# Kernel tuning notes

Measured on AMD Instinct MI355X. Metric: run time of the kernel, lower is better.

Reference implementation:

```python
import jax, jax.numpy as jnp
import numpy as np

H = 512   # layer_size
D = 5     # dim
B = 64
T = 512
EPS = 1e-3  # Keras BatchNormalization default epsilon


def _p(key, shape, scale=0.05):
    return jax.random.normal(key, shape, dtype=jnp.float32) * scale


def setup_inputs() -> dict:
    key = jax.random.key(0)
    ks = jax.random.split(key, 32)
    inp = {
        "x": jax.random.normal(ks[0], (B, T, D), dtype=jnp.float32),
        # LSTM 1 (input D)
        "W1": _p(ks[1], (D, 4 * H)), "U1": _p(ks[2], (H, 4 * H)), "b1": jnp.zeros((4 * H,), jnp.float32),
        # BatchNorm on H features (inference: moving stats)
        "g1": jnp.ones((H,), jnp.float32), "be1": jnp.zeros((H,), jnp.float32),
        "m1": _p(ks[3], (H,), 0.1), "v1": jnp.ones((H,), jnp.float32) + jax.random.uniform(ks[4], (H,)) * 0.1,
        # LSTM 2 (input H)
        "W2": _p(ks[5], (H, 4 * H)), "U2": _p(ks[6], (H, 4 * H)), "b2": jnp.zeros((4 * H,), jnp.float32),
        # LSTM 3 (input H, returns last state only)
        "W3": _p(ks[7], (H, 4 * H)), "U3": _p(ks[8], (H, 4 * H)), "b3": jnp.zeros((4 * H,), jnp.float32),
        # dense head y
        "d1w": _p(ks[9], (H, 32)), "d1b": jnp.zeros((32,), jnp.float32),
        "g2": jnp.ones((32,), jnp.float32), "be2": jnp.zeros((32,), jnp.float32),
        "m2": _p(ks[10], (32,), 0.1), "v2": jnp.ones((32,), jnp.float32) + jax.random.uniform(ks[11], (32,)) * 0.1,
        "d2w": _p(ks[12], (32, 16)), "d2b": jnp.zeros((16,), jnp.float32),
        "hw": _p(ks[13], (16, 1)), "hb": jnp.zeros((1,), jnp.float32),
        # dense head z
        "d4w": _p(ks[14], (H, 128)), "d4b": jnp.zeros((128,), jnp.float32),
        "d5w": _p(ks[15], (128, 64)), "d5b": jnp.zeros((64,), jnp.float32),
        "rw": _p(ks[16], (64, D)), "rb": jnp.zeros((D,), jnp.float32),
    }
    return inp


def lstm(x, W, U, b):
    """Keras LSTM, gate order i,f,c,o. x: [B,T,din] -> (seq [B,T,H], h_T, c_T)."""
    xz = jnp.einsum('btd,dk->btk', x, W) + b  # precompute input projections [B,T,4H]

    def step(carry, xz_t):
        h, c = carry
        z = xz_t + h @ U
        i, f, g, o = jnp.split(z, 4, axis=-1)
        i = jax.nn.sigmoid(i)
        f = jax.nn.sigmoid(f)
        g = jnp.tanh(g)
        o = jax.nn.sigmoid(o)
        c = f * c + i * g
        h = o * jnp.tanh(c)
        return (h, c), h

    b_ = x.shape[0]
    h0 = jnp.zeros((b_, U.shape[0]), x.dtype)
    (hT, cT), hs = jax.lax.scan(step, (h0, h0), jnp.swapaxes(xz, 0, 1))
    return jnp.swapaxes(hs, 0, 1), hT, cT


def bn_inf(x, g, b, m, v):
    return (x - m) * (g / jnp.sqrt(v + EPS)) + b


def reference(x, W1, U1, b1, g1, be1, m1, v1, W2, U2, b2, W3, U3, b3,
              d1w, d1b, g2, be2, m2, v2, d2w, d2b, hw, hb,
              d4w, d4b, d5w, d5b, rw, rb):
    # inference: GaussianNoise / Dropout are identity
    x1, h1, s1 = lstm(x, W1, U1, b1)          # [B,T,H]
    xr = bn_inf(x1, g1, be1, m1, v1)
    x2, h2, s2 = lstm(xr, W2, U2, b2)         # [B,T,H]
    xs = x1 + x2                               # residual Add
    _, h3, s3 = lstm(xs, W3, U3, b3)           # last hidden state [B,H]
    xlast = h3
    # head y
    y = xlast @ d1w + d1b
    y = bn_inf(y, g2, be2, m2, v2)
    y = y @ d2w + d2b
    y = jax.nn.sigmoid(y @ hw + hb)            # [B,1]
    # head z
    z = xlast @ d4w + d4b
    z = z @ d5w + d5b
    z = z @ rw + rb                            # [B,D]
    return (y, z)
```

## Files before the change

### kernel.cpp

```cpp
#include <hip/hip_runtime.h>
#include <hip/hip_bf16.h>

typedef short bf16x8 __attribute__((ext_vector_type(8)));
typedef float f32x4 __attribute__((ext_vector_type(4)));
typedef unsigned short u16;
typedef unsigned int u32;
typedef unsigned long long u64;

#define EPSBN 1e-3f

__device__ __forceinline__ u16 f2b(float f){
  unsigned u = __float_as_uint(f);
  return (u16)((u + 0x7fffu + ((u >> 16) & 1u)) >> 16);
}
__device__ __forceinline__ float b2f(u16 v){ return __uint_as_float(((unsigned)v) << 16); }
__device__ __forceinline__ float sigm(float x){ return 1.f/(1.f + __expf(-x)); }
__device__ __forceinline__ float tanhx(float x){ return 2.f/(1.f + __expf(-2.f*x)) - 1.f; }

union U64x2 { u64 q[2]; bf16x8 v; };


__global__ void prep_sv(const float* __restrict__ g1, const float* __restrict__ be1,
                        const float* __restrict__ m1, const float* __restrict__ v1,
                        float* __restrict__ s, float* __restrict__ tv){
  int k = blockIdx.x*256 + threadIdx.x;
  if (k < 512){
    float sv = g1[k] * rsqrtf(v1[k] + EPSBN);
    s[k] = sv;
    tv[k] = be1[k] - m1[k]*sv;
  }
}

__global__ void prep_b2p(const float* __restrict__ W2, const float* __restrict__ b2,
                         const float* __restrict__ tv, float* __restrict__ out){
  int col = blockIdx.x*256 + threadIdx.x;
  float acc = b2[col];
  for (int k=0;k<512;++k) acc += tv[k] * W2[(size_t)k*2048 + col];
  out[col] = acc;
}

__global__ void transpose_pack(const float* __restrict__ in, const float* __restrict__ scale,
                               u16* __restrict__ out){
  __shared__ float tile[64][65];
  int k0 = blockIdx.x * 64;
  int c0 = blockIdx.y * 64;
  int t = threadIdx.x;
  int cc = t & 63, kk0 = (t >> 6) * 16;
  #pragma unroll
  for (int i=0;i<16;++i){
    float v = in[(size_t)(k0 + kk0 + i)*2048 + c0 + cc];
    if (scale) v *= scale[k0 + kk0 + i];
    tile[kk0 + i][cc] = v;
  }
  __syncthreads();
  int cc2 = t >> 2, kp = t & 3;
  int col = c0 + cc2;
  int hcol = col & 511;
  int row = (hcol >> 5)*128 + (col >> 9)*32 + ((hcol >> 4) & 1)*16 + (col & 15);
  bf16x8 v0, v1;
  #pragma unroll
  for (int i=0;i<8;++i){
    v0[i] = (short)f2b(tile[kp*16 + i][cc2]);
    v1[i] = (short)f2b(tile[kp*16 + 8 + i][cc2]);
  }
  u16* dst = out + (size_t)row*512 + k0 + kp*16;
  *(bf16x8*)dst = v0;
  *(bf16x8*)(dst + 8) = v1;
}

__global__ void pack_w1(const float* __restrict__ W1, u16* __restrict__ out){
  int r = blockIdx.x*256 + threadIdx.x;
  int wg = r >> 7, q = (r >> 5) & 3, jt = (r >> 4) & 1, jj = r & 15;
  int col = q*512 + wg*32 + jt*16 + jj;
  #pragma unroll
  for (int k=0;k<32;++k)
    out[(size_t)r*32 + k] = (k < 5) ? f2b(W1[(size_t)k*2048 + col]) : (u16)0;
}

__global__ void pack_x(const float* __restrict__ x, u16* __restrict__ out){
  int i = blockIdx.x*256 + threadIdx.x;
  int k = i & 31;
  int bt = i >> 5;
  out[i] = (k < 5) ? f2b(x[(size_t)bt*5 + k]) : (u16)0;
}

__global__ void __launch_bounds__(256, 1) scan_all(
    const u16* __restrict__ Ure1, const u16* __restrict__ Ure2, const u16* __restrict__ Ure3,
    const u16* __restrict__ W1p,  const u16* __restrict__ W2p,  const u16* __restrict__ W3p,
    const u16* __restrict__ xpad,
    const float* __restrict__ b1, const float* __restrict__ b2p, const float* __restrict__ b3,
    u32* __restrict__ hbuf_all,
    u32* __restrict__ x1seq,
    u32* __restrict__ xsseq,
    float* __restrict__ h3out, u32* __restrict__ cnt)
{
  const int bid = blockIdx.x;
  const int phase = bid >> 6;
  const int b6 = bid & 63;
  const int g = b6 & 3, wg = b6 >> 2;
  const int tid = threadIdx.x;
  const int w = tid >> 6, l = tid & 63;
  const int lm = l & 15, lh = l >> 4;
  const int bg0 = g * 16;
  const int b_own = tid & 15, jl = tid >> 4;
  const int pb = tid >> 4, pj = tid & 15;

  const u16* Ure  = phase == 0 ? Ure1 : (phase == 1 ? Ure2 : Ure3);
  const u16* Wre  = phase == 0 ? W1p  : (phase == 1 ? W2p  : W3p);
  const float* bias = phase == 0 ? b1 : (phase == 1 ? b2p : b3);
  u32* hbuf32 = hbuf_all + (size_t)phase * 32768;
  u32* seqout = phase == 0 ? x1seq : (phase == 1 ? xsseq : nullptr);
  const u32* upseq = phase == 1 ? x1seq : (phase == 2 ? xsseq : nullptr);

  u32* cq  = cnt + (phase*4 + g)*64;
  u32* sq_ = cq + 32;
  u32* upq = (phase > 0) ? cnt + ((phase-1)*4 + g)*64 + 32 : nullptr;

  bf16x8 aU[8][4];
  #pragma unroll
  for (int q=0;q<4;++q)
    #pragma unroll
    for (int jt=0;jt<2;++jt){
      const u16* up = Ure + (size_t)(wg*128 + q*32 + jt*16 + lm)*512 + w*128 + lh*8;
      #pragma unroll
      for (int ks=0;ks<4;++ks) aU[q*2+jt][ks] = *(const bf16x8*)(up + ks*32);
    }
  bf16x8 aW[8][4];
  if (phase == 0){
    #pragma unroll
    for (int q=0;q<4;++q)
      #pragma unroll
      for (int jt=0;jt<2;++jt)
        aW[q*2+jt][0] = *(const bf16x8*)(Wre + (size_t)(wg*128 + q*32 + jt*16 + lm)*32 + lh*8);
  } else {
    #pragma unroll
    for (int q=0;q<4;++q)
      #pragma unroll
      for (int jt=0;jt<2;++jt){
        const u16* wp = Wre + (size_t)(wg*128 + q*32 + jt*16 + lm)*512 + w*128 + lh*8;
        #pragma unroll
        for (int ks=0;ks<4;++ks) aW[q*2+jt][ks] = *(const bf16x8*)(wp + ks*32);
      }
  }

  float bias_g[4][2];
  #pragma unroll
  for (int q=0;q<4;++q){
    bias_g[q][0] = bias[q*512 + wg*32 + jl];
    bias_g[q][1] = bias[q*512 + wg*32 + jl + 16];
  }

  float cs0 = 0.f, cs1 = 0.f;

  __shared__ float zex[8][4][16][17];
  __shared__ __align__(8) u16 hsh[16][32];
  __shared__ __align__(8) u16 xsh[16][32];
  __shared__ u32 x1w[16][16];

  const u64* hbase = (const u64*)hbuf32;

  for (int t=0; t<512; ++t){
    f32x4 acc[8] = {};

    if (phase == 0){
      if (w == 0){
        bf16x8 bx = *(const bf16x8*)(xpad + ((size_t)(bg0+lm)*512 + t)*32 + lh*8);
        #pragma unroll
        for (int i=0;i<8;++i)
          acc[i] = __builtin_amdgcn_mfma_f32_16x16x32_bf16(aW[i][0], bx, acc[i], 0,0,0);
      }
    } else {
      if (tid == 0){
        const u32 target = (u32)(16*(t+1));
        while (__hip_atomic_load(upq, __ATOMIC_RELAXED, __HIP_MEMORY_SCOPE_AGENT) < target) {}
      }
      __syncthreads();
      if (phase == 1){
        u32 rv = __hip_atomic_load(upseq + ((size_t)(bg0+pb)*512 + t)*256 + wg*16 + pj,
                                   __ATOMIC_RELAXED, __HIP_MEMORY_SCOPE_AGENT);
        x1w[pb][pj] = rv;
      }
      const u64* xp = (const u64*)upseq + ((size_t)(bg0+lm)*512 + t)*128 + w*32 + lh*2;
      U64x2 xq[4];
      #pragma unroll
      for (int ks=0;ks<4;++ks){
        xq[ks].q[0] = __hip_atomic_load(xp + ks*8,     __ATOMIC_RELAXED, __HIP_MEMORY_SCOPE_AGENT);
        xq[ks].q[1] = __hip_atomic_load(xp + ks*8 + 1, __ATOMIC_RELAXED, __HIP_MEMORY_SCOPE_AGENT);
      }
      #pragma unroll
      for (int ks=0;ks<4;++ks){
        #pragma unroll
        for (int i=0;i<8;++i)
          acc[i] = __builtin_amdgcn_mfma_f32_16x16x32_bf16(aW[i][ks], xq[ks].v, acc[i], 0,0,0);
      }
    }

    if (tid == 0){
      const u32 target = (u32)(16*t);
      while (__hip_atomic_load(cq, __ATOMIC_RELAXED, __HIP_MEMORY_SCOPE_AGENT) < target) {}
    }
    __syncthreads();

    {
      const u64* hp = hbase + (size_t)(((t+1)&1)*64 + bg0 + lm)*128 + w*32 + lh*2;
      U64x2 hq[4];
      #pragma unroll
      for (int ks=0;ks<4;++ks){
        hq[ks].q[0] = __hip_atomic_load(hp + ks*8,     __ATOMIC_RELAXED, __HIP_MEMORY_SCOPE_AGENT);
        hq[ks].q[1] = __hip_atomic_load(hp + ks*8 + 1, __ATOMIC_RELAXED, __HIP_MEMORY_SCOPE_AGENT);
      }
      #pragma unroll
      for (int ks=0;ks<4;++ks){
        #pragma unroll
        for (int i=0;i<8;++i)
          acc[i] = __builtin_amdgcn_mfma_f32_16x16x32_bf16(aU[i][ks], hq[ks].v, acc[i], 0,0,0);
      }
    }

    #pragma unroll
    for (int i=0;i<8;++i){
      #pragma unroll
      for (int r=0;r<4;++r)
        zex[i][w][lh*4 + r][lm] = acc[i][r];
    }
    __syncthreads();

    float hv0, hv1;
    {
      float zv[4][2];
      #pragma unroll
      for (int q=0;q<4;++q){
        #pragma unroll
        for (int s2=0;s2<2;++s2)
          zv[q][s2] = zex[q*2+s2][0][jl][b_own] + zex[q*2+s2][1][jl][b_own]
                    + zex[q*2+s2][2][jl][b_own] + zex[q*2+s2][3][jl][b_own] + bias_g[q][s2];
      }
      float iv = sigm(zv[0][0]), fv = sigm(zv[1][0]), gv = tanhx(zv[2][0]), ov = sigm(zv[3][0]);
      cs0 = fv * cs0 + iv * gv;
      hv0 = ov * tanhx(cs0);
      iv = sigm(zv[0][1]); fv = sigm(zv[1][1]); gv = tanhx(zv[2][1]); ov = sigm(zv[3][1]);
      cs1 = fv * cs1 + iv * gv;
      hv1 = ov * tanhx(cs1);
    }

    hsh[b_own][jl]      = f2b(hv0);
    hsh[b_own][jl + 16] = f2b(hv1);
    if (phase == 1){
      u32 w0 = x1w[b_own][jl >> 1], w1 = x1w[b_own][8 + (jl >> 1)];
      float x1r0 = b2f((u16)((jl & 1) ? (w0 >> 16) : (w0 & 0xffffu)));
      float x1r1 = b2f((u16)((jl & 1) ? (w1 >> 16) : (w1 & 0xffffu)));
      xsh[b_own][jl]      = f2b(x1r0 + hv0);
      xsh[b_own][jl + 16] = f2b(x1r1 + hv1);
    }
    if (phase == 2 && t == 511){
      h3out[(size_t)(bg0+b_own)*512 + wg*32 + jl]      = hv0;
      h3out[(size_t)(bg0+b_own)*512 + wg*32 + jl + 16] = hv1;
    }
    __syncthreads();

    u32 pv = (u32)hsh[pb][2*pj] | ((u32)hsh[pb][2*pj+1] << 16);
    __hip_atomic_store(hbuf32 + (size_t)((t&1)*64 + bg0 + pb)*256 + wg*16 + pj, pv,
                       __ATOMIC_RELAXED, __HIP_MEMORY_SCOPE_AGENT);
    if (phase == 0){
      __hip_atomic_store(seqout + ((size_t)(bg0+pb)*512 + t)*256 + wg*16 + pj, pv,
                         __ATOMIC_RELAXED, __HIP_MEMORY_SCOPE_AGENT);
    } else if (phase == 1){
      u32 sv = (u32)xsh[pb][2*pj] | ((u32)xsh[pb][2*pj+1] << 16);
      __hip_atomic_store(seqout + ((size_t)(bg0+pb)*512 + t)*256 + wg*16 + pj, sv,
                         __ATOMIC_RELAXED, __HIP_MEMORY_SCOPE_AGENT);
    }
    asm volatile("s_waitcnt vmcnt(0)" ::: "memory");
    __syncthreads();
    if (tid == 0){
      __hip_atomic_fetch_add(cq, 1u, __ATOMIC_RELAXED, __HIP_MEMORY_SCOPE_AGENT);
      if (phase < 2)
        __hip_atomic_fetch_add(sq_, 1u, __ATOMIC_RELAXED, __HIP_MEMORY_SCOPE_AGENT);
    }
  }
}

__global__ void __launch_bounds__(256) head_k(
    const float* __restrict__ h3,
    const float* __restrict__ d1w, const float* __restrict__ d1b,
    const float* __restrict__ g2, const float* __restrict__ be2,
    const float* __restrict__ m2, const float* __restrict__ v2,
    const float* __restrict__ d2w, const float* __restrict__ d2b,
    const float* __restrict__ hw, const float* __restrict__ hb,
    const float* __restrict__ d4w, const float* __restrict__ d4b,
    const float* __restrict__ d5w, const float* __restrict__ d5b,
    const float* __restrict__ rw, const float* __restrict__ rb,
    float* __restrict__ out)
{
  __shared__ float hl[512];
  __shared__ float a1[32], a2[16], c1[128], c2[64];
  int b = blockIdx.x, t = threadIdx.x;
  for (int i=t; i<512; i+=256) hl[i] = h3[(size_t)b*512 + i];
  __syncthreads();
  if (t < 32){
    float acc = d1b[t];
    for (int k=0;k<512;++k) acc += hl[k] * d1w[(size_t)k*32 + t];
    a1[t] = (acc - m2[t]) * (g2[t] * rsqrtf(v2[t] + EPSBN)) + be2[t];
  } else if (t >= 128){
    int i = t - 128;
    float acc = d4b[i];
    for (int k=0;k<512;++k) acc += hl[k] * d4w[(size_t)k*128 + i];
    c1[i] = acc;
  }
  __syncthreads();
  if (t < 16){
    float acc = d2b[t];
    for (int k=0;k<32;++k) acc += a1[k] * d2w[k*16 + t];
    a2[t] = acc;
  } else if (t >= 64 && t < 128){
    int i = t - 64;
    float acc = d5b[i];
    for (int k=0;k<128;++k) acc += c1[k] * d5w[k*64 + i];
    c2[i] = acc;
  }
  __syncthreads();
  if (t == 0){
    float acc = hb[0];
    for (int k=0;k<16;++k) acc += a2[k] * hw[k];
    out[b] = 1.f/(1.f + __expf(-acc));
  } else if (t >= 32 && t < 37){
    int i = t - 32;
    float acc = rb[i];
    for (int k=0;k<64;++k) acc += c2[k] * rw[k*5 + i];
    out[64 + b*5 + i] = acc;
  }
}

extern "C" void kernel_launch(void* const* d_in, const int* in_sizes, int n_in,
                              void* d_out, int out_size, void* d_ws, size_t ws_size,
                              hipStream_t stream)
{
  const float* x   = (const float*)d_in[0];
  const float* W1  = (const float*)d_in[1];
  const float* U1  = (const float*)d_in[2];
  const float* b1  = (const float*)d_in[3];
  const float* g1  = (const float*)d_in[4];
  const float* be1 = (const float*)d_in[5];
  const float* m1  = (const float*)d_in[6];
  const float* v1  = (const float*)d_in[7];
  const float* W2  = (const float*)d_in[8];
  const float* U2  = (const float*)d_in[9];
  const float* b2  = (const float*)d_in[10];
  const float* W3  = (const float*)d_in[11];
  const float* U3  = (const float*)d_in[12];
  const float* b3  = (const float*)d_in[13];
  const float* d1w = (const float*)d_in[14];
  const float* d1b = (const float*)d_in[15];
  const float* g2  = (const float*)d_in[16];
  const float* be2 = (const float*)d_in[17];
  const float* m2  = (const float*)d_in[18];
  const float* v2  = (const float*)d_in[19];
  const float* d2w = (const float*)d_in[20];
  const float* d2b = (const float*)d_in[21];
  const float* hw  = (const float*)d_in[22];
  const float* hb  = (const float*)d_in[23];
  const float* d4w = (const float*)d_in[24];
  const float* d4b = (const float*)d_in[25];
  const float* d5w = (const float*)d_in[26];
  const float* d5b = (const float*)d_in[27];
  const float* rw  = (const float*)d_in[28];
  const float* rb  = (const float*)d_in[29];

  char* ws = (char*)d_ws;
  constexpr size_t SZ_W   = 2048ull*512*2;
  constexpr size_t o_Ure1 = 0;
  constexpr size_t o_Ure2 = o_Ure1 + SZ_W;
  constexpr size_t o_Ure3 = o_Ure2 + SZ_W;
  constexpr size_t o_W2p  = o_Ure3 + SZ_W;
  constexpr size_t o_W3p  = o_W2p + SZ_W;
  constexpr size_t o_W1p  = o_W3p + SZ_W;
  constexpr size_t o_xpad = o_W1p + 2048ull*32*2;
  constexpr size_t o_b2p  = o_xpad + 64ull*512*32*2;
  constexpr size_t o_s    = o_b2p + 2048ull*4;
  constexpr size_t o_tv   = o_s + 512ull*4;
  constexpr size_t o_h3   = o_tv + 512ull*4;
  constexpr size_t o_h    = o_h3 + 64ull*512*4;
  constexpr size_t SZ_HP  = 2ull*64*256*4;
  constexpr size_t SZ_H   = 3*SZ_HP;
  constexpr size_t o_cnt  = o_h + SZ_H;
  constexpr size_t SZ_CNT = 3ull*4*64*4;
  constexpr size_t o_x1   = o_cnt + 4096;
  constexpr size_t o_xs   = o_x1 + 64ull*512*512*2;

  u16* Ure1 = (u16*)(ws + o_Ure1);
  u16* Ure2 = (u16*)(ws + o_Ure2);
  u16* Ure3 = (u16*)(ws + o_Ure3);
  u16* W2p  = (u16*)(ws + o_W2p);
  u16* W3p  = (u16*)(ws + o_W3p);
  u16* W1p  = (u16*)(ws + o_W1p);
  u16* xpad = (u16*)(ws + o_xpad);
  u32* x1p  = (u32*)(ws + o_x1);
  u32* xsp  = (u32*)(ws + o_xs);

  hipMemsetAsync(ws + o_h, 0, SZ_H + SZ_CNT, stream);

  prep_sv<<<dim3(2), dim3(256), 0, stream>>>(g1, be1, m1, v1, (float*)(ws+o_s), (float*)(ws+o_tv));
  transpose_pack<<<dim3(8,32), dim3(256), 0, stream>>>(U1, nullptr, Ure1);
  transpose_pack<<<dim3(8,32), dim3(256), 0, stream>>>(U2, nullptr, Ure2);
  transpose_pack<<<dim3(8,32), dim3(256), 0, stream>>>(U3, nullptr, Ure3);
  transpose_pack<<<dim3(8,32), dim3(256), 0, stream>>>(W3, nullptr, W3p);
  transpose_pack<<<dim3(8,32), dim3(256), 0, stream>>>(W2, (const float*)(ws+o_s), W2p);
  prep_b2p<<<dim3(8), dim3(256), 0, stream>>>(W2, b2, (const float*)(ws+o_tv), (float*)(ws+o_b2p));
  pack_w1<<<dim3(8), dim3(256), 0, stream>>>(W1, W1p);
  pack_x<<<dim3(4096), dim3(256), 0, stream>>>(x, xpad);

  scan_all<<<dim3(192), dim3(256), 0, stream>>>(
      Ure1, Ure2, Ure3, W1p, W2p, W3p, xpad,
      b1, (const float*)(ws+o_b2p), b3,
      (u32*)(ws+o_h), x1p, xsp,
      (float*)(ws+o_h3), (u32*)(ws+o_cnt));

  head_k<<<dim3(64), dim3(256), 0, stream>>>((const float*)(ws+o_h3),
      d1w, d1b, g2, be2, m2, v2, d2w, d2b, hw, hb, d4w, d4b, d5w, d5b, rw, rb,
      (float*)d_out);
}
```

Baseline: 2.338 ms.

## Replace shared atomic counters with per-wave flag stores and wave-level polling

Replaces the single per-group atomic counter, which thread 0 incremented and polled behind workgroup barriers, with per-wave flag slots. Each wave stores its timestep and waits only on the specific flags whose data it reads, with all lanes polling in parallel under __all. This removes contended atomic read-modify-writes and two __syncthreads per step from the critical recurrence path. The risks are more polling traffic and subtle memory-ordering issues, since the stores are relaxed and the cross-wave dependency mapping must be exactly right.

```diff
diff --git a/kernel.cpp b/kernel.cpp
--- a/kernel.cpp
+++ b/kernel.cpp
@@ -84,6 +84,10 @@
   out[i] = (k < 5) ? f2b(x[(size_t)bt*5 + k]) : (u16)0;
 }
 
+__device__ __forceinline__ void poll_flags(const u32* p, u32 target, bool act){
+  while (!__all((!act) | (__hip_atomic_load(p, __ATOMIC_RELAXED, __HIP_MEMORY_SCOPE_AGENT) >= target))) {}
+}
+
 __global__ void __launch_bounds__(256, 1) scan_all(
     const u16* __restrict__ Ure1, const u16* __restrict__ Ure2, const u16* __restrict__ Ure3,
     const u16* __restrict__ W1p,  const u16* __restrict__ W2p,  const u16* __restrict__ W3p,
@@ -92,7 +96,7 @@
     u32* __restrict__ hbuf_all,
     u32* __restrict__ x1seq,
     u32* __restrict__ xsseq,
-    float* __restrict__ h3out, u32* __restrict__ cnt)
+    float* __restrict__ h3out, u32* __restrict__ flags_base)
 {
   const int bid = blockIdx.x;
   const int phase = bid >> 6;
@@ -112,9 +116,13 @@
   u32* seqout = phase == 0 ? x1seq : (phase == 1 ? xsseq : nullptr);
   const u32* upseq = phase == 1 ? x1seq : (phase == 2 ? xsseq : nullptr);
 
-  u32* cq  = cnt + (phase*4 + g)*64;
-  u32* sq_ = cq + 32;
-  u32* upq = (phase > 0) ? cnt + ((phase-1)*4 + g)*64 + 32 : nullptr;
+  u32* flg  = flags_base + (phase*4 + g)*64;
+  const u32* upflg = (phase > 0) ? flags_base + ((phase-1)*4 + g)*64 : nullptr;
+
+  const u32* hpoll = flg + 16*w + (l & 15);
+  const u32* xpoll = (phase > 0)
+      ? ((l < 16) ? upflg + 16*w + l : upflg + 4*wg + w)
+      : nullptr;
 
   bf16x8 aU[8][4];
   #pragma unroll
@@ -170,11 +178,7 @@
           acc[i] = __builtin_amdgcn_mfma_f32_16x16x32_bf16(aW[i][0], bx, acc[i], 0,0,0);
       }
     } else {
-      if (tid == 0){
-        const u32 target = (u32)(16*(t+1));
-        while (__hip_atomic_load(upq, __ATOMIC_RELAXED, __HIP_MEMORY_SCOPE_AGENT) < target) {}
-      }
-      __syncthreads();
+      poll_flags(xpoll, (u32)(t+1), l < 20);
       if (phase == 1){
         u32 rv = __hip_atomic_load(upseq + ((size_t)(bg0+pb)*512 + t)*256 + wg*16 + pj,
                                    __ATOMIC_RELAXED, __HIP_MEMORY_SCOPE_AGENT);
@@ -195,11 +199,7 @@
       }
     }
 
-    if (tid == 0){
-      const u32 target = (u32)(16*t);
-      while (__hip_atomic_load(cq, __ATOMIC_RELAXED, __HIP_MEMORY_SCOPE_AGENT) < target) {}
-    }
-    __syncthreads();
+    poll_flags(hpoll, (u32)t, true);
 
     {
       const u64* hp = hbase + (size_t)(((t+1)&1)*64 + bg0 + lm)*128 + w*32 + lh*2;
@@ -270,12 +270,9 @@
                          __ATOMIC_RELAXED, __HIP_MEMORY_SCOPE_AGENT);
     }
     asm volatile("s_waitcnt vmcnt(0)" ::: "memory");
-    __syncthreads();
-    if (tid == 0){
-      __hip_atomic_fetch_add(cq, 1u, __ATOMIC_RELAXED, __HIP_MEMORY_SCOPE_AGENT);
-      if (phase < 2)
-        __hip_atomic_fetch_add(sq_, 1u, __ATOMIC_RELAXED, __HIP_MEMORY_SCOPE_AGENT);
-    }
+    if (l == 0)
+      __hip_atomic_store(flg + wg*4 + w, (u32)(t+1),
+                         __ATOMIC_RELAXED, __HIP_MEMORY_SCOPE_AGENT);
   }
 }
 
```

Result: slower. 2.579 ms (+10.3%).

## Replace per-step counter barrier with tagged hidden-state words polled by consumers

Applied to the files above, without the earlier changes.

Each bf16 hidden value is now stored together with a 16-bit timestep tag in one 32-bit word. Consumer waves spin directly on the tagged data until every tag matches the expected step, which removes the intra-layer atomic counter wait, its syncthreads and the counter increment for the recurrent dependency. The counter and its fence are kept only for the cross-layer sequence handoff, and phase 2 drops them entirely. The cost is twice the h-buffer traffic and repeated polling reads. Shared arrays are also padded to change bank mapping.

```diff
diff --git a/kernel.cpp b/kernel.cpp
--- a/kernel.cpp
+++ b/kernel.cpp
@@ -18,6 +18,7 @@
 __device__ __forceinline__ float tanhx(float x){ return 2.f/(1.f + __expf(-2.f*x)) - 1.f; }
 
 union U64x2 { u64 q[2]; bf16x8 v; };
+union BP    { u32 p[4]; bf16x8 v; };
 
 
 __global__ void prep_sv(const float* __restrict__ g1, const float* __restrict__ be1,
@@ -108,13 +109,12 @@
   const u16* Ure  = phase == 0 ? Ure1 : (phase == 1 ? Ure2 : Ure3);
   const u16* Wre  = phase == 0 ? W1p  : (phase == 1 ? W2p  : W3p);
   const float* bias = phase == 0 ? b1 : (phase == 1 ? b2p : b3);
-  u32* hbuf32 = hbuf_all + (size_t)phase * 32768;
+  u32* hbuf32 = hbuf_all + (size_t)phase * 65536;
   u32* seqout = phase == 0 ? x1seq : (phase == 1 ? xsseq : nullptr);
   const u32* upseq = phase == 1 ? x1seq : (phase == 2 ? xsseq : nullptr);
 
   u32* cq  = cnt + (phase*4 + g)*64;
-  u32* sq_ = cq + 32;
-  u32* upq = (phase > 0) ? cnt + ((phase-1)*4 + g)*64 + 32 : nullptr;
+  const u32* upq = (phase > 0) ? cnt + ((phase-1)*4 + g)*64 : nullptr;
 
   bf16x8 aU[8][4];
   #pragma unroll
@@ -152,12 +152,12 @@
 
   float cs0 = 0.f, cs1 = 0.f;
 
-  __shared__ float zex[8][4][16][17];
-  __shared__ __align__(8) u16 hsh[16][32];
-  __shared__ __align__(8) u16 xsh[16][32];
-  __shared__ u32 x1w[16][16];
-
-  const u64* hbase = (const u64*)hbuf32;
+  __shared__ float zex[8][4][16][18];
+  __shared__ u16 hsh[16][34];
+  __shared__ u16 xsh[16][34];
+  __shared__ u32 x1w[16][17];
+
+  const u64 tagmask = 0x0000FFFF0000FFFFull;
 
   for (int t=0; t<512; ++t){
     f32x4 acc[8] = {};
@@ -195,25 +195,38 @@
       }
     }
 
-    if (tid == 0){
-      const u32 target = (u32)(16*t);
-      while (__hip_atomic_load(cq, __ATOMIC_RELAXED, __HIP_MEMORY_SCOPE_AGENT) < target) {}
-    }
-    __syncthreads();
-
-    {
-      const u64* hp = hbase + (size_t)(((t+1)&1)*64 + bg0 + lm)*128 + w*32 + lh*2;
-      U64x2 hq[4];
+    if (t > 0){
+      const int slot = (t+1) & 1;
+      const u64* hp = (const u64*)hbuf32
+                    + (size_t)(slot*64 + bg0 + lm)*256 + w*64 + lh*4;
+      const u32 tg = (u32)t;
+      const u64 want = (u64)tg | ((u64)tg << 32);
+      u64 raw[16];
+      bool ok;
+      do {
+        #pragma unroll
+        for (int ks=0;ks<4;++ks)
+          #pragma unroll
+          for (int qq=0;qq<4;++qq)
+            raw[ks*4+qq] = __hip_atomic_load(hp + ks*16 + qq,
+                                             __ATOMIC_RELAXED, __HIP_MEMORY_SCOPE_AGENT);
+        u64 bad = 0;
+        #pragma unroll
+        for (int i=0;i<16;++i) bad |= (raw[i] & tagmask) ^ want;
+        ok = __all(bad == 0);
+      } while (!ok);
       #pragma unroll
       for (int ks=0;ks<4;++ks){
-        hq[ks].q[0] = __hip_atomic_load(hp + ks*8,     __ATOMIC_RELAXED, __HIP_MEMORY_SCOPE_AGENT);
-        hq[ks].q[1] = __hip_atomic_load(hp + ks*8 + 1, __ATOMIC_RELAXED, __HIP_MEMORY_SCOPE_AGENT);
-      }
-      #pragma unroll
-      for (int ks=0;ks<4;++ks){
+        BP bp;
+        #pragma unroll
+        for (int qq=0;qq<4;++qq){
+          u32 lo = (u32)raw[ks*4+qq];
+          u32 hi = (u32)(raw[ks*4+qq] >> 32);
+          bp.p[qq] = (lo >> 16) | (hi & 0xFFFF0000u);
+        }
         #pragma unroll
         for (int i=0;i<8;++i)
-          acc[i] = __builtin_amdgcn_mfma_f32_16x16x32_bf16(aU[i][ks], hq[ks].v, acc[i], 0,0,0);
+          acc[i] = __builtin_amdgcn_mfma_f32_16x16x32_bf16(aU[i][ks], bp.v, acc[i], 0,0,0);
       }
     }
 
@@ -258,23 +271,26 @@
     }
     __syncthreads();
 
-    u32 pv = (u32)hsh[pb][2*pj] | ((u32)hsh[pb][2*pj+1] << 16);
-    __hip_atomic_store(hbuf32 + (size_t)((t&1)*64 + bg0 + pb)*256 + wg*16 + pj, pv,
-                       __ATOMIC_RELAXED, __HIP_MEMORY_SCOPE_AGENT);
-    if (phase == 0){
-      __hip_atomic_store(seqout + ((size_t)(bg0+pb)*512 + t)*256 + wg*16 + pj, pv,
+    {
+      const int pslot = t & 1;
+      const u32 tagv = (u32)(t + 1);
+      u32 w0 = ((u32)hsh[pb][2*pj]     << 16) | tagv;
+      u32 w1 = ((u32)hsh[pb][2*pj + 1] << 16) | tagv;
+      __hip_atomic_store((u64*)(hbuf32 + (size_t)(pslot*64 + bg0 + pb)*512 + wg*32) + pj,
+                         (u64)w0 | ((u64)w1 << 32),
                          __ATOMIC_RELAXED, __HIP_MEMORY_SCOPE_AGENT);
-    } else if (phase == 1){
-      u32 sv = (u32)xsh[pb][2*pj] | ((u32)xsh[pb][2*pj+1] << 16);
+    }
+
+    if (phase < 2){
+      u32 sv;
+      if (phase == 0) sv = (u32)hsh[pb][2*pj] | ((u32)hsh[pb][2*pj+1] << 16);
+      else            sv = (u32)xsh[pb][2*pj] | ((u32)xsh[pb][2*pj+1] << 16);
       __hip_atomic_store(seqout + ((size_t)(bg0+pb)*512 + t)*256 + wg*16 + pj, sv,
                          __ATOMIC_RELAXED, __HIP_MEMORY_SCOPE_AGENT);
-    }
-    asm volatile("s_waitcnt vmcnt(0)" ::: "memory");
-    __syncthreads();
-    if (tid == 0){
-      __hip_atomic_fetch_add(cq, 1u, __ATOMIC_RELAXED, __HIP_MEMORY_SCOPE_AGENT);
-      if (phase < 2)
-        __hip_atomic_fetch_add(sq_, 1u, __ATOMIC_RELAXED, __HIP_MEMORY_SCOPE_AGENT);
+      asm volatile("s_waitcnt vmcnt(0)" ::: "memory");
+      __syncthreads();
+      if (tid == 0)
+        __hip_atomic_fetch_add(cq, 1u, __ATOMIC_RELAXED, __HIP_MEMORY_SCOPE_AGENT);
     }
   }
 }
@@ -379,10 +395,9 @@
   constexpr size_t o_tv   = o_s + 512ull*4;
   constexpr size_t o_h3   = o_tv + 512ull*4;
   constexpr size_t o_h    = o_h3 + 64ull*512*4;
-  constexpr size_t SZ_HP  = 2ull*64*256*4;
+  constexpr size_t SZ_HP  = 2ull*64*512*4;
   constexpr size_t SZ_H   = 3*SZ_HP;
   constexpr size_t o_cnt  = o_h + SZ_H;
-  constexpr size_t SZ_CNT = 3ull*4*64*4;
   constexpr size_t o_x1   = o_cnt + 4096;
   constexpr size_t o_xs   = o_x1 + 64ull*512*512*2;
 
@@ -396,7 +411,7 @@
   u32* x1p  = (u32*)(ws + o_x1);
   u32* xsp  = (u32*)(ws + o_xs);
 
-  hipMemsetAsync(ws + o_h, 0, SZ_H + SZ_CNT, stream);
+  hipMemsetAsync(ws + o_h, 0, SZ_H + 4096, stream);
 
   prep_sv<<<dim3(2), dim3(256), 0, stream>>>(g1, be1, m1, v1, (float*)(ws+o_s), (float*)(ws+o_tv));
   transpose_pack<<<dim3(8,32), dim3(256), 0, stream>>>(U1, nullptr, Ure1);
```

Result: slower. 2.892 ms (+23.7%).

## Split LSTM scan blocks into eight waves and streamline cross-block signaling

Applied to the files above, without the earlier changes.

Each scan block now runs 512 threads (eight waves). Each wave handles one of the two j-tiles for one k-slice, so per-wave MFMA chains and register weight tiles are halved. All threads now poll the step counters directly instead of one thread polling before a barrier. The extra shared staging of h and xs is removed, and packed h, residual and sequence values are stored straight from the gate threads. The separate sequence counter and the explicit vmcnt wait before signaling are dropped. This shortens the per-step critical path, but it risks memory-ordering visibility issues and adds polling traffic from many lanes.

```diff
diff --git a/kernel.cpp b/kernel.cpp
--- a/kernel.cpp
+++ b/kernel.cpp
@@ -84,7 +84,11 @@
   out[i] = (k < 5) ? f2b(x[(size_t)bt*5 + k]) : (u16)0;
 }
 
-__global__ void __launch_bounds__(256, 1) scan_all(
+__device__ __forceinline__ void pollge(const u32* p, u32 target){
+  while (__hip_atomic_load(p, __ATOMIC_RELAXED, __HIP_MEMORY_SCOPE_AGENT) < target) {}
+}
+
+__global__ void __launch_bounds__(512, 2) scan_all(
     const u16* __restrict__ Ure1, const u16* __restrict__ Ure2, const u16* __restrict__ Ure3,
     const u16* __restrict__ W1p,  const u16* __restrict__ W2p,  const u16* __restrict__ W3p,
     const u16* __restrict__ xpad,
@@ -100,10 +104,11 @@
   const int g = b6 & 3, wg = b6 >> 2;
   const int tid = threadIdx.x;
   const int w = tid >> 6, l = tid & 63;
-  const int lm = l & 15, lh = l >> 4;
+  const int lm = l & 15, lh = (l >> 4) & 3;
+  const int kp = w & 3, jt = w >> 2;
   const int bg0 = g * 16;
-  const int b_own = tid & 15, jl = tid >> 4;
-  const int pb = tid >> 4, pj = tid & 15;
+  const int jp = tid & 15, gb = (tid >> 4) & 15;
+  const int jt2 = jp >> 3;
 
   const u16* Ure  = phase == 0 ? Ure1 : (phase == 1 ? Ure2 : Ure3);
   const u16* Wre  = phase == 0 ? W1p  : (phase == 1 ? W2p  : W3p);
@@ -113,74 +118,63 @@
   const u32* upseq = phase == 1 ? x1seq : (phase == 2 ? xsseq : nullptr);
 
   u32* cq  = cnt + (phase*4 + g)*64;
-  u32* sq_ = cq + 32;
-  u32* upq = (phase > 0) ? cnt + ((phase-1)*4 + g)*64 + 32 : nullptr;
-
-  bf16x8 aU[8][4];
+  const u32* upq = (phase > 0) ? cnt + ((phase-1)*4 + g)*64 : nullptr;
+
+  bf16x8 aU[4][4];
   #pragma unroll
-  for (int q=0;q<4;++q)
+  for (int q=0;q<4;++q){
+    const u16* up = Ure + (size_t)(wg*128 + q*32 + jt*16 + lm)*512 + kp*128 + lh*8;
     #pragma unroll
-    for (int jt=0;jt<2;++jt){
-      const u16* up = Ure + (size_t)(wg*128 + q*32 + jt*16 + lm)*512 + w*128 + lh*8;
-      #pragma unroll
-      for (int ks=0;ks<4;++ks) aU[q*2+jt][ks] = *(const bf16x8*)(up + ks*32);
-    }
-  bf16x8 aW[8][4];
+    for (int ks=0;ks<4;++ks) aU[q][ks] = *(const bf16x8*)(up + ks*32);
+  }
+  bf16x8 aW[4][4];
+  bf16x8 aW1[4];
   if (phase == 0){
-    #pragma unroll
-    for (int q=0;q<4;++q)
-      #pragma unroll
-      for (int jt=0;jt<2;++jt)
-        aW[q*2+jt][0] = *(const bf16x8*)(Wre + (size_t)(wg*128 + q*32 + jt*16 + lm)*32 + lh*8);
+    if (kp == 0){
+      #pragma unroll
+      for (int q=0;q<4;++q)
+        aW1[q] = *(const bf16x8*)(Wre + (size_t)(wg*128 + q*32 + jt*16 + lm)*32 + lh*8);
+    }
   } else {
     #pragma unroll
-    for (int q=0;q<4;++q)
-      #pragma unroll
-      for (int jt=0;jt<2;++jt){
-        const u16* wp = Wre + (size_t)(wg*128 + q*32 + jt*16 + lm)*512 + w*128 + lh*8;
-        #pragma unroll
-        for (int ks=0;ks<4;++ks) aW[q*2+jt][ks] = *(const bf16x8*)(wp + ks*32);
-      }
-  }
-
-  float bias_g[4][2];
-  #pragma unroll
-  for (int q=0;q<4;++q){
-    bias_g[q][0] = bias[q*512 + wg*32 + jl];
-    bias_g[q][1] = bias[q*512 + wg*32 + jl + 16];
+    for (int q=0;q<4;++q){
+      const u16* wp = Wre + (size_t)(wg*128 + q*32 + jt*16 + lm)*512 + kp*128 + lh*8;
+      #pragma unroll
+      for (int ks=0;ks<4;++ks) aW[q][ks] = *(const bf16x8*)(wp + ks*32);
+    }
+  }
+
+  float bias0[4], bias1[4];
+  if (tid < 256){
+    #pragma unroll
+    for (int q=0;q<4;++q){
+      bias0[q] = bias[q*512 + wg*32 + 2*jp];
+      bias1[q] = bias[q*512 + wg*32 + 2*jp + 1];
+    }
   }
 
   float cs0 = 0.f, cs1 = 0.f;
 
-  __shared__ float zex[8][4][16][17];
-  __shared__ __align__(8) u16 hsh[16][32];
-  __shared__ __align__(8) u16 xsh[16][32];
-  __shared__ u32 x1w[16][16];
-
+  __shared__ float zex[8][4][16][18];
   const u64* hbase = (const u64*)hbuf32;
 
   for (int t=0; t<512; ++t){
-    f32x4 acc[8] = {};
+    f32x4 acc[4] = {};
+    u32 rv = 0;
 
     if (phase == 0){
-      if (w == 0){
+      if (kp == 0){
         bf16x8 bx = *(const bf16x8*)(xpad + ((size_t)(bg0+lm)*512 + t)*32 + lh*8);
         #pragma unroll
-        for (int i=0;i<8;++i)
-          acc[i] = __builtin_amdgcn_mfma_f32_16x16x32_bf16(aW[i][0], bx, acc[i], 0,0,0);
+        for (int q=0;q<4;++q)
+          acc[q] = __builtin_amdgcn_mfma_f32_16x16x32_bf16(aW1[q], bx, acc[q], 0,0,0);
       }
     } else {
-      if (tid == 0){
-        const u32 target = (u32)(16*(t+1));
-        while (__hip_atomic_load(upq, __ATOMIC_RELAXED, __HIP_MEMORY_SCOPE_AGENT) < target) {}
-      }
-      __syncthreads();
-      if (phase == 1){
-        u32 rv = __hip_atomic_load(upseq + ((size_t)(bg0+pb)*512 + t)*256 + wg*16 + pj,
-                                   __ATOMIC_RELAXED, __HIP_MEMORY_SCOPE_AGENT);
-        x1w[pb][pj] = rv;
-      }
-      const u64* xp = (const u64*)upseq + ((size_t)(bg0+lm)*512 + t)*128 + w*32 + lh*2;
+      pollge(upq, (u32)(16*(t+1)));
+      if (phase == 1 && tid < 256)
+        rv = __hip_atomic_load(upseq + ((size_t)(bg0+gb)*512 + t)*256 + wg*16 + jp,
+                               __ATOMIC_RELAXED, __HIP_MEMORY_SCOPE_AGENT);
+      const u64* xp = (const u64*)upseq + ((size_t)(bg0+lm)*512 + t)*128 + kp*32 + lh*2;
       U64x2 xq[4];
       #pragma unroll
       for (int ks=0;ks<4;++ks){
@@ -190,19 +184,14 @@
       #pragma unroll
       for (int ks=0;ks<4;++ks){
         #pragma unroll
-        for (int i=0;i<8;++i)
-          acc[i] = __builtin_amdgcn_mfma_f32_16x16x32_bf16(aW[i][ks], xq[ks].v, acc[i], 0,0,0);
-      }
-    }
-
-    if (tid == 0){
-      const u32 target = (u32)(16*t);
-      while (__hip_atomic_load(cq, __ATOMIC_RELAXED, __HIP_MEMORY_SCOPE_AGENT) < target) {}
-    }
-    __syncthreads();
-
+        for (int q=0;q<4;++q)
+          acc[q] = __builtin_amdgcn_mfma_f32_16x16x32_bf16(aW[q][ks], xq[ks].v, acc[q], 0,0,0);
+      }
+    }
+
+    pollge(cq, (u32)(16*t));
     {
-      const u64* hp = hbase + (size_t)(((t+1)&1)*64 + bg0 + lm)*128 + w*32 + lh*2;
+      const u64* hp = hbase + (size_t)(((t+1)&1)*64 + bg0 + lm)*128 + kp*32 + lh*2;
       U64x2 hq[4];
       #pragma unroll
       for (int ks=0;ks<4;++ks){
@@ -212,70 +201,57 @@
       #pragma unroll
       for (int ks=0;ks<4;++ks){
         #pragma unroll
-        for (int i=0;i<8;++i)
-          acc[i] = __builtin_amdgcn_mfma_f32_16x16x32_bf16(aU[i][ks], hq[ks].v, acc[i], 0,0,0);
+        for (int q=0;q<4;++q)
+          acc[q] = __builtin_amdgcn_mfma_f32_16x16x32_bf16(aU[q][ks], hq[ks].v, acc[q], 0,0,0);
       }
     }
 
     #pragma unroll
-    for (int i=0;i<8;++i){
+    for (int q=0;q<4;++q){
       #pragma unroll
       for (int r=0;r<4;++r)
-        zex[i][w][lh*4 + r][lm] = acc[i][r];
+        zex[q*2+jt][kp][lh*4 + r][lm] = acc[q][r];
     }
     __syncthreads();
 
-    float hv0, hv1;
-    {
-      float zv[4][2];
+    if (tid < 256){
+      const int r0 = (2*jp) & 15, r1 = r0 + 1;
+      float zv0[4], zv1[4];
       #pragma unroll
       for (int q=0;q<4;++q){
-        #pragma unroll
-        for (int s2=0;s2<2;++s2)
-          zv[q][s2] = zex[q*2+s2][0][jl][b_own] + zex[q*2+s2][1][jl][b_own]
-                    + zex[q*2+s2][2][jl][b_own] + zex[q*2+s2][3][jl][b_own] + bias_g[q][s2];
-      }
-      float iv = sigm(zv[0][0]), fv = sigm(zv[1][0]), gv = tanhx(zv[2][0]), ov = sigm(zv[3][0]);
+        const int ti = q*2 + jt2;
+        zv0[q] = zex[ti][0][r0][gb] + zex[ti][1][r0][gb]
+               + zex[ti][2][r0][gb] + zex[ti][3][r0][gb] + bias0[q];
+        zv1[q] = zex[ti][0][r1][gb] + zex[ti][1][r1][gb]
+               + zex[ti][2][r1][gb] + zex[ti][3][r1][gb] + bias1[q];
+      }
+      float iv = sigm(zv0[0]), fv = sigm(zv0[1]), gv = tanhx(zv0[2]), ov = sigm(zv0[3]);
       cs0 = fv * cs0 + iv * gv;
-      hv0 = ov * tanhx(cs0);
-      iv = sigm(zv[0][1]); fv = sigm(zv[1][1]); gv = tanhx(zv[2][1]); ov = sigm(zv[3][1]);
+      float hv0 = ov * tanhx(cs0);
+      iv = sigm(zv1[0]); fv = sigm(zv1[1]); gv = tanhx(zv1[2]); ov = sigm(zv1[3]);
       cs1 = fv * cs1 + iv * gv;
-      hv1 = ov * tanhx(cs1);
-    }
-
-    hsh[b_own][jl]      = f2b(hv0);
-    hsh[b_own][jl + 16] = f2b(hv1);
-    if (phase == 1){
-      u32 w0 = x1w[b_own][jl >> 1], w1 = x1w[b_own][8 + (jl >> 1)];
-      float x1r0 = b2f((u16)((jl & 1) ? (w0 >> 16) : (w0 & 0xffffu)));
-      float x1r1 = b2f((u16)((jl & 1) ? (w1 >> 16) : (w1 & 0xffffu)));
-      xsh[b_own][jl]      = f2b(x1r0 + hv0);
-      xsh[b_own][jl + 16] = f2b(x1r1 + hv1);
-    }
-    if (phase == 2 && t == 511){
-      h3out[(size_t)(bg0+b_own)*512 + wg*32 + jl]      = hv0;
-      h3out[(size_t)(bg0+b_own)*512 + wg*32 + jl + 16] = hv1;
+      float hv1 = ov * tanhx(cs1);
+
+      const u32 pw = (u32)f2b(hv0) | ((u32)f2b(hv1) << 16);
+      __hip_atomic_store(hbuf32 + (size_t)((t&1)*64 + bg0 + gb)*256 + wg*16 + jp, pw,
+                         __ATOMIC_RELAXED, __HIP_MEMORY_SCOPE_AGENT);
+      if (phase == 0){
+        __hip_atomic_store(seqout + ((size_t)(bg0+gb)*512 + t)*256 + wg*16 + jp, pw,
+                           __ATOMIC_RELAXED, __HIP_MEMORY_SCOPE_AGENT);
+      } else if (phase == 1){
+        float x1r0 = b2f((u16)(rv & 0xffffu));
+        float x1r1 = b2f((u16)(rv >> 16));
+        u32 sv = (u32)f2b(x1r0 + hv0) | ((u32)f2b(x1r1 + hv1) << 16);
+        __hip_atomic_store(seqout + ((size_t)(bg0+gb)*512 + t)*256 + wg*16 + jp, sv,
+                           __ATOMIC_RELAXED, __HIP_MEMORY_SCOPE_AGENT);
+      } else if (t == 511){
+        h3out[(size_t)(bg0+gb)*512 + wg*32 + 2*jp]     = hv0;
+        h3out[(size_t)(bg0+gb)*512 + wg*32 + 2*jp + 1] = hv1;
+      }
     }
     __syncthreads();
-
-    u32 pv = (u32)hsh[pb][2*pj] | ((u32)hsh[pb][2*pj+1] << 16);
-    __hip_atomic_store(hbuf32 + (size_t)((t&1)*64 + bg0 + pb)*256 + wg*16 + pj, pv,
-                       __ATOMIC_RELAXED, __HIP_MEMORY_SCOPE_AGENT);
-    if (phase == 0){
-      __hip_atomic_store(seqout + ((size_t)(bg0+pb)*512 + t)*256 + wg*16 + pj, pv,
-                         __ATOMIC_RELAXED, __HIP_MEMORY_SCOPE_AGENT);
-    } else if (phase == 1){
-      u32 sv = (u32)xsh[pb][2*pj] | ((u32)xsh[pb][2*pj+1] << 16);
-      __hip_atomic_store(seqout + ((size_t)(bg0+pb)*512 + t)*256 + wg*16 + pj, sv,
-                         __ATOMIC_RELAXED, __HIP_MEMORY_SCOPE_AGENT);
-    }
-    asm volatile("s_waitcnt vmcnt(0)" ::: "memory");
-    __syncthreads();
-    if (tid == 0){
+    if (tid == 0)
       __hip_atomic_fetch_add(cq, 1u, __ATOMIC_RELAXED, __HIP_MEMORY_SCOPE_AGENT);
-      if (phase < 2)
-        __hip_atomic_fetch_add(sq_, 1u, __ATOMIC_RELAXED, __HIP_MEMORY_SCOPE_AGENT);
-    }
   }
 }
 
@@ -382,7 +358,6 @@
   constexpr size_t SZ_HP  = 2ull*64*256*4;
   constexpr size_t SZ_H   = 3*SZ_HP;
   constexpr size_t o_cnt  = o_h + SZ_H;
-  constexpr size_t SZ_CNT = 3ull*4*64*4;
   constexpr size_t o_x1   = o_cnt + 4096;
   constexpr size_t o_xs   = o_x1 + 64ull*512*512*2;
 
@@ -396,7 +371,7 @@
   u32* x1p  = (u32*)(ws + o_x1);
   u32* xsp  = (u32*)(ws + o_xs);
 
-  hipMemsetAsync(ws + o_h, 0, SZ_H + SZ_CNT, stream);
+  hipMemsetAsync(ws + o_h, 0, SZ_H + 4096, stream);
 
   prep_sv<<<dim3(2), dim3(256), 0, stream>>>(g1, be1, m1, v1, (float*)(ws+o_s), (float*)(ws+o_tv));
   transpose_pack<<<dim3(8,32), dim3(256), 0, stream>>>(U1, nullptr, Ure1);
@@ -408,7 +383,7 @@
   pack_w1<<<dim3(8), dim3(256), 0, stream>>>(W1, W1p);
   pack_x<<<dim3(4096), dim3(256), 0, stream>>>(x, xpad);
 
-  scan_all<<<dim3(192), dim3(256), 0, stream>>>(
+  scan_all<<<dim3(192), dim3(512), 0, stream>>>(
       Ure1, Ure2, Ure3, W1p, W2p, W3p, xpad,
       b1, (const float*)(ws+o_b2p), b3,
       (u32*)(ws+o_h), x1p, xsp,
```

Result: slower. 2.629 ms (+12.5%).
